# Performance work log

Hardware: AMD Instinct MI355X
Metric: run time of the kernel (lower is better)

The kernel has to match this reference:

```python
import jax, jax.numpy as jnp
import numpy as np

B, N, M, D, H = 2, 512, 512, 128, 256
EPS = 1e-5


def _layernorm(x, g, b):
    mu = jnp.mean(x, axis=-1, keepdims=True)
    var = jnp.mean(jnp.square(x - mu), axis=-1, keepdims=True)
    return (x - mu) * jax.lax.rsqrt(var + EPS) * g + b


def setup_inputs() -> dict:
    key = jax.random.key(0)
    ks = jax.random.split(key, 12)
    X = jax.random.normal(ks[0], (B, N, D), dtype=jnp.float32)
    Y = jax.random.normal(ks[1], (B, M, D), dtype=jnp.float32)
    mask = jax.random.randint(ks[2], (B, N, M), 0, 2).astype(jnp.int32)
    s_in = 1.0 / np.sqrt(2 * D)
    s_h = 1.0 / np.sqrt(H)
    s_d = 1.0 / np.sqrt(D)
    # edge-net Linear(2D, H) split into Y-half and X-half (pairs = cat([Y, X]))
    W1y = jax.random.normal(ks[3], (D, H), dtype=jnp.float32) * s_in
    W1x = jax.random.normal(ks[4], (D, H), dtype=jnp.float32) * s_in
    b1 = jnp.zeros((H,), dtype=jnp.float32)
    W2 = jax.random.normal(ks[5], (H, D), dtype=jnp.float32) * s_h
    b2 = jnp.zeros((D,), dtype=jnp.float32)
    Wf1 = jax.random.normal(ks[6], (D, H), dtype=jnp.float32) * s_d
    bf1 = jnp.zeros((H,), dtype=jnp.float32)
    Wf2 = jax.random.normal(ks[7], (H, D), dtype=jnp.float32) * s_h
    bf2 = jnp.zeros((D,), dtype=jnp.float32)
    g0 = jnp.ones((D,), dtype=jnp.float32)
    be0 = jnp.zeros((D,), dtype=jnp.float32)
    g1 = jnp.ones((D,), dtype=jnp.float32)
    be1 = jnp.zeros((D,), dtype=jnp.float32)
    return {"X": X, "Y": Y, "mask": mask, "W1y": W1y, "W1x": W1x, "b1": b1,
            "W2": W2, "b2": b2, "Wf1": Wf1, "bf1": bf1, "Wf2": Wf2, "bf2": bf2,
            "g0": g0, "be0": be0, "g1": g1, "be1": be1}


def reference(X, Y, mask, W1y, W1x, b1, W2, b2, Wf1, bf1, Wf2, bf2, g0, be0, g1, be1):
    # pairs[b,n,m] = concat(Y[b,m], X[b,n]); Linear on concat == sum of two GEMMs,
    # so avoid materializing the [B,N,M,2D] pairs tensor.
    hy = jnp.einsum('bmd,dh->bmh', Y, W1y)          # [B,M,H]
    hx = jnp.einsum('bnd,dh->bnh', X, W1x)          # [B,N,H]
    h = jax.nn.relu(hy[:, None, :, :] + hx[:, :, None, :] + b1)   # [B,N,M,H]
    E = jnp.einsum('bnmh,hd->bnmd', h, W2) + b2     # [B,N,M,D]
    E = E * mask[..., None].astype(E.dtype)         # masked sum-pool over M
    Z = X + jnp.sum(E, axis=2)                      # residual, [B,N,D]
    Z = _layernorm(Z, g0, be0)
    Z = Z + jax.nn.relu(Z @ Wf1 + bf1) @ Wf2 + bf2  # residual MLP
    Z = _layernorm(Z, g1, be1)
    return Z
```

## Files before the change

kernel.cpp:

```cpp
#include <hip/hip_runtime.h>

#define BB 2
#define NN 512
#define MM 512
#define DD 128
#define HH 256

__global__ __launch_bounds__(256) void k_inproj(
    const float* __restrict__ X, const float* __restrict__ Y,
    const float* __restrict__ W1x, const float* __restrict__ W1y,
    const float* __restrict__ b1,
    float* __restrict__ hx, float* __restrict__ hy)
{
    __shared__ float sr[DD][8];
    int blk = blockIdx.x;
    bool isX = blk < 128;
    const float* src = isX ? X : Y;
    const float* W   = isX ? W1x : W1y;
    float* dst       = isX ? hx : hy;
    int row0 = (isX ? blk : blk - 128) * 8;
    int t = threadIdx.x;

    for (int k = 0; k < 4; ++k) {
        int idx = t + k * 256;
        int r = idx >> 7, d = idx & 127;
        sr[d][r] = src[(row0 + r) * DD + d];
    }
    __syncthreads();

    float bias = isX ? b1[t] : 0.0f;
    float acc[8];
#pragma unroll
    for (int i = 0; i < 8; ++i) acc[i] = bias;

    for (int d = 0; d < DD; ++d) {
        float w = W[d * HH + t];
        float4 a0 = *(const float4*)&sr[d][0];
        float4 a1 = *(const float4*)&sr[d][4];
        acc[0] = fmaf(a0.x, w, acc[0]);
        acc[1] = fmaf(a0.y, w, acc[1]);
        acc[2] = fmaf(a0.z, w, acc[2]);
        acc[3] = fmaf(a0.w, w, acc[3]);
        acc[4] = fmaf(a1.x, w, acc[4]);
        acc[5] = fmaf(a1.y, w, acc[5]);
        acc[6] = fmaf(a1.z, w, acc[6]);
        acc[7] = fmaf(a1.w, w, acc[7]);
    }
#pragma unroll
    for (int i = 0; i < 8; ++i) dst[(row0 + i) * HH + t] = acc[i];
}

__global__ __launch_bounds__(256) void k_main(
    const float* __restrict__ hx, const float* __restrict__ hy,
    const int* __restrict__ mask, float* __restrict__ Spart)
{
    __shared__ float mf[256][4];
    int blk   = blockIdx.x;
    int ms    = blk & 1;
    int ntile = (blk >> 1) & 127;
    int b     = blk >> 8;
    int n0    = ntile * 4;
    int t     = threadIdx.x;

    const int* mrow = mask + (b * NN + n0) * MM + ms * 256;
#pragma unroll
    for (int i = 0; i < 4; ++i)
        mf[t][i] = (float)mrow[i * MM + t];
    __syncthreads();

    float hxv[4], acc[4] = {0.f, 0.f, 0.f, 0.f};
#pragma unroll
    for (int i = 0; i < 4; ++i)
        hxv[i] = hx[(b * NN + n0 + i) * HH + t];

    const float* hyp = hy + (b * MM + ms * 256) * HH + t;
#pragma unroll 4
    for (int m = 0; m < 256; ++m) {
        float hyv = hyp[m * HH];
        float4 m4 = *(const float4*)&mf[m][0];
        float t0 = fmaxf(hxv[0] + hyv, 0.f);
        float t1 = fmaxf(hxv[1] + hyv, 0.f);
        float t2 = fmaxf(hxv[2] + hyv, 0.f);
        float t3 = fmaxf(hxv[3] + hyv, 0.f);
        acc[0] = fmaf(t0, m4.x, acc[0]);
        acc[1] = fmaf(t1, m4.y, acc[1]);
        acc[2] = fmaf(t2, m4.z, acc[2]);
        acc[3] = fmaf(t3, m4.w, acc[3]);
    }
    float* sp = Spart + (size_t)ms * (BB * NN * HH) + (b * NN + n0) * HH + t;
#pragma unroll
    for (int i = 0; i < 4; ++i) sp[i * HH] = acc[i];
}

__global__ __launch_bounds__(256) void k_epi(
    const float* __restrict__ X, const int* __restrict__ mask,
    const float* __restrict__ Spart,
    const float* __restrict__ W2, const float* __restrict__ b2,
    const float* __restrict__ Wf1, const float* __restrict__ bf1,
    const float* __restrict__ Wf2, const float* __restrict__ bf2,
    const float* __restrict__ g0, const float* __restrict__ be0,
    const float* __restrict__ g1, const float* __restrict__ be1,
    float* __restrict__ out)
{
    __shared__ float sS[4][HH];
    __shared__ float szp[4][DD];
    __shared__ float sz[4][DD];
    __shared__ float su[4][HH];
    __shared__ float spart[2][4][DD];
    __shared__ float scnt[4];

    int blk = blockIdx.x;
    int b   = blk >> 7;
    int n0  = (blk & 127) * 4;
    int t   = threadIdx.x;
    int wave = t >> 6, lane = t & 63;

#pragma unroll
    for (int i = 0; i < 4; ++i)
        sS[i][t] = Spart[(b * NN + n0 + i) * HH + t]
                 + Spart[(size_t)(BB * NN * HH) + (b * NN + n0 + i) * HH + t];

    {
        const int* mrow = mask + (b * NN + n0 + wave) * MM;
        int c = 0;
#pragma unroll
        for (int k = 0; k < 8; ++k) c += mrow[lane + k * 64];
#pragma unroll
        for (int off = 32; off; off >>= 1) c += __shfl_down(c, off);
        if (lane == 0) scnt[wave] = (float)c;
    }
    __syncthreads();

    {
        int d = t & 127, half = t >> 7;
        float a0 = 0, a1 = 0, a2 = 0, a3 = 0;
        int hbase = half * 128;
        for (int h = 0; h < 128; ++h) {
            float w = W2[(hbase + h) * DD + d];
            a0 = fmaf(sS[0][hbase + h], w, a0);
            a1 = fmaf(sS[1][hbase + h], w, a1);
            a2 = fmaf(sS[2][hbase + h], w, a2);
            a3 = fmaf(sS[3][hbase + h], w, a3);
        }
        spart[half][0][d] = a0; spart[half][1][d] = a1;
        spart[half][2][d] = a2; spart[half][3][d] = a3;
    }
    __syncthreads();
#pragma unroll
    for (int k = 0; k < 2; ++k) {
        int o = t + k * 256, i = o >> 7, d = o & 127;
        szp[i][d] = spart[0][i][d] + spart[1][i][d]
                  + X[(b * NN + n0 + i) * DD + d] + scnt[i] * b2[d];
    }
    __syncthreads();

    {
        float v0 = szp[wave][lane], v1 = szp[wave][lane + 64];
        float s = v0 + v1, q = v0 * v0 + v1 * v1;
#pragma unroll
        for (int off = 32; off; off >>= 1) { s += __shfl_down(s, off); q += __shfl_down(q, off); }
        s = __shfl(s, 0); q = __shfl(q, 0);
        float mu   = s * (1.0f / 128.0f);
        float var  = q * (1.0f / 128.0f) - mu * mu;
        float rstd = rsqrtf(var + 1e-5f);
        sz[wave][lane]      = (v0 - mu) * rstd * g0[lane]      + be0[lane];
        sz[wave][lane + 64] = (v1 - mu) * rstd * g0[lane + 64] + be0[lane + 64];
    }
    __syncthreads();

    {
        float bias = bf1[t];
        float a0 = bias, a1 = bias, a2 = bias, a3 = bias;
        for (int d = 0; d < DD; ++d) {
            float w = Wf1[d * HH + t];
            a0 = fmaf(sz[0][d], w, a0);
            a1 = fmaf(sz[1][d], w, a1);
            a2 = fmaf(sz[2][d], w, a2);
            a3 = fmaf(sz[3][d], w, a3);
        }
        su[0][t] = fmaxf(a0, 0.f);
        su[1][t] = fmaxf(a1, 0.f);
        su[2][t] = fmaxf(a2, 0.f);
        su[3][t] = fmaxf(a3, 0.f);
    }
    __syncthreads();

    {
        int d = t & 127, half = t >> 7;
        float a0 = 0, a1 = 0, a2 = 0, a3 = 0;
        int hbase = half * 128;
        for (int h = 0; h < 128; ++h) {
            float w = Wf2[(hbase + h) * DD + d];
            a0 = fmaf(su[0][hbase + h], w, a0);
            a1 = fmaf(su[1][hbase + h], w, a1);
            a2 = fmaf(su[2][hbase + h], w, a2);
            a3 = fmaf(su[3][hbase + h], w, a3);
        }
        spart[half][0][d] = a0; spart[half][1][d] = a1;
        spart[half][2][d] = a2; spart[half][3][d] = a3;
    }
    __syncthreads();
#pragma unroll
    for (int k = 0; k < 2; ++k) {
        int o = t + k * 256, i = o >> 7, d = o & 127;
        szp[i][d] = sz[i][d] + spart[0][i][d] + spart[1][i][d] + bf2[d];
    }
    __syncthreads();

    {
        float v0 = szp[wave][lane], v1 = szp[wave][lane + 64];
        float s = v0 + v1, q = v0 * v0 + v1 * v1;
#pragma unroll
        for (int off = 32; off; off >>= 1) { s += __shfl_down(s, off); q += __shfl_down(q, off); }
        s = __shfl(s, 0); q = __shfl(q, 0);
        float mu   = s * (1.0f / 128.0f);
        float var  = q * (1.0f / 128.0f) - mu * mu;
        float rstd = rsqrtf(var + 1e-5f);
        int row = (b * NN + n0 + wave) * DD;
        out[row + lane]      = (v0 - mu) * rstd * g1[lane]      + be1[lane];
        out[row + lane + 64] = (v1 - mu) * rstd * g1[lane + 64] + be1[lane + 64];
    }
}

extern "C" void kernel_launch(void* const* d_in, const int* in_sizes, int n_in,
                              void* d_out, int out_size, void* d_ws, size_t ws_size,
                              hipStream_t stream)
{
    const float* X    = (const float*)d_in[0];
    const float* Y    = (const float*)d_in[1];
    const int*   mask = (const int*)d_in[2];
    const float* W1y  = (const float*)d_in[3];
    const float* W1x  = (const float*)d_in[4];
    const float* b1   = (const float*)d_in[5];
    const float* W2   = (const float*)d_in[6];
    const float* b2   = (const float*)d_in[7];
    const float* Wf1  = (const float*)d_in[8];
    const float* bf1  = (const float*)d_in[9];
    const float* Wf2  = (const float*)d_in[10];
    const float* bf2  = (const float*)d_in[11];
    const float* g0   = (const float*)d_in[12];
    const float* be0  = (const float*)d_in[13];
    const float* g1   = (const float*)d_in[14];
    const float* be1  = (const float*)d_in[15];
    float* out = (float*)d_out;

    float* ws = (float*)d_ws;
    float* hx = ws;
    float* hy = ws + BB * NN * HH;
    float* Sp = ws + 2 * BB * NN * HH;

    k_inproj<<<256, 256, 0, stream>>>(X, Y, W1x, W1y, b1, hx, hy);
    k_main  <<<512, 256, 0, stream>>>(hx, hy, mask, Sp);
    k_epi   <<<256, 256, 0, stream>>>(X, mask, Sp, W2, b2, Wf1, bf1, Wf2, bf2,
                                      g0, be0, g1, be1, out);
}
```

Before: 135.4 us.

## Split work finer across all three kernels to raise block and thread counts

The input projection now computes 4 rows per block instead of 8, doubling the block count. The main pairwise reduction splits M into four chunks instead of two, doubling its blocks. The epilogue uses 512 threads and splits each reduction dimension across more thread groups, combining the pieces through a shared scratch buffer. The aim is more waves in flight to hide latency on a many-CU GPU, at the cost of more partial-sum traffic and a larger workspace for the four Spart slices.

```diff
diff --git a/kernel.cpp b/kernel.cpp
--- a/kernel.cpp
+++ b/kernel.cpp
@@ -12,16 +12,17 @@
     const float* __restrict__ b1,
     float* __restrict__ hx, float* __restrict__ hy)
 {
-    __shared__ float sr[DD][8];
+    __shared__ float sr[DD][4];
     int blk = blockIdx.x;
-    bool isX = blk < 128;
+    bool isX = blk < 256;
     const float* src = isX ? X : Y;
     const float* W   = isX ? W1x : W1y;
     float* dst       = isX ? hx : hy;
-    int row0 = (isX ? blk : blk - 128) * 8;
+    int row0 = (isX ? blk : blk - 256) * 4;
     int t = threadIdx.x;
 
-    for (int k = 0; k < 4; ++k) {
+#pragma unroll
+    for (int k = 0; k < 2; ++k) {
         int idx = t + k * 256;
         int r = idx >> 7, d = idx & 127;
         sr[d][r] = src[(row0 + r) * DD + d];
@@ -29,43 +30,41 @@
     __syncthreads();
 
     float bias = isX ? b1[t] : 0.0f;
-    float acc[8];
-#pragma unroll
-    for (int i = 0; i < 8; ++i) acc[i] = bias;
-
+    float a0 = bias, a1 = bias, a2 = bias, a3 = bias;
+
+#pragma unroll 16
     for (int d = 0; d < DD; ++d) {
         float w = W[d * HH + t];
-        float4 a0 = *(const float4*)&sr[d][0];
-        float4 a1 = *(const float4*)&sr[d][4];
-        acc[0] = fmaf(a0.x, w, acc[0]);
-        acc[1] = fmaf(a0.y, w, acc[1]);
-        acc[2] = fmaf(a0.z, w, acc[2]);
-        acc[3] = fmaf(a0.w, w, acc[3]);
-        acc[4] = fmaf(a1.x, w, acc[4]);
-        acc[5] = fmaf(a1.y, w, acc[5]);
-        acc[6] = fmaf(a1.z, w, acc[6]);
-        acc[7] = fmaf(a1.w, w, acc[7]);
-    }
-#pragma unroll
-    for (int i = 0; i < 8; ++i) dst[(row0 + i) * HH + t] = acc[i];
+        float4 a = *(const float4*)&sr[d][0];
+        a0 = fmaf(a.x, w, a0);
+        a1 = fmaf(a.y, w, a1);
+        a2 = fmaf(a.z, w, a2);
+        a3 = fmaf(a.w, w, a3);
+    }
+    dst[(row0 + 0) * HH + t] = a0;
+    dst[(row0 + 1) * HH + t] = a1;
+    dst[(row0 + 2) * HH + t] = a2;
+    dst[(row0 + 3) * HH + t] = a3;
 }
 
 __global__ __launch_bounds__(256) void k_main(
     const float* __restrict__ hx, const float* __restrict__ hy,
     const int* __restrict__ mask, float* __restrict__ Spart)
 {
-    __shared__ float mf[256][4];
+    __shared__ float mf[128][4];
     int blk   = blockIdx.x;
-    int ms    = blk & 1;
-    int ntile = (blk >> 1) & 127;
-    int b     = blk >> 8;
+    int ms    = blk & 3;
+    int ntile = (blk >> 2) & 127;
+    int b     = blk >> 9;
     int n0    = ntile * 4;
     int t     = threadIdx.x;
 
-    const int* mrow = mask + (b * NN + n0) * MM + ms * 256;
-#pragma unroll
-    for (int i = 0; i < 4; ++i)
-        mf[t][i] = (float)mrow[i * MM + t];
+    if (t < 128) {
+        const int* mrow = mask + (b * NN + n0) * MM + ms * 128 + t;
+#pragma unroll
+        for (int i = 0; i < 4; ++i)
+            mf[t][i] = (float)mrow[i * MM];
+    }
     __syncthreads();
 
     float hxv[4], acc[4] = {0.f, 0.f, 0.f, 0.f};
@@ -73,9 +72,9 @@
     for (int i = 0; i < 4; ++i)
         hxv[i] = hx[(b * NN + n0 + i) * HH + t];
 
-    const float* hyp = hy + (b * MM + ms * 256) * HH + t;
-#pragma unroll 4
-    for (int m = 0; m < 256; ++m) {
+    const float* hyp = hy + (b * MM + ms * 128) * HH + t;
+#pragma unroll 8
+    for (int m = 0; m < 128; ++m) {
         float hyv = hyp[m * HH];
         float4 m4 = *(const float4*)&mf[m][0];
         float t0 = fmaxf(hxv[0] + hyv, 0.f);
@@ -92,7 +91,7 @@
     for (int i = 0; i < 4; ++i) sp[i * HH] = acc[i];
 }
 
-__global__ __launch_bounds__(256) void k_epi(
+__global__ __launch_bounds__(512) void k_epi(
     const float* __restrict__ X, const int* __restrict__ mask,
     const float* __restrict__ Spart,
     const float* __restrict__ W2, const float* __restrict__ b2,
@@ -106,7 +105,7 @@
     __shared__ float szp[4][DD];
     __shared__ float sz[4][DD];
     __shared__ float su[4][HH];
-    __shared__ float spart[2][4][DD];
+    __shared__ float scratch[2048];
     __shared__ float scnt[4];
 
     int blk = blockIdx.x;
@@ -116,11 +115,17 @@
     int wave = t >> 6, lane = t & 63;
 
 #pragma unroll
-    for (int i = 0; i < 4; ++i)
-        sS[i][t] = Spart[(b * NN + n0 + i) * HH + t]
-                 + Spart[(size_t)(BB * NN * HH) + (b * NN + n0 + i) * HH + t];
-
-    {
+    for (int k = 0; k < 2; ++k) {
+        int idx = t + k * 512;
+        int r = idx >> 8, h = idx & 255;
+        size_t base = (size_t)(b * NN + n0 + r) * HH + h;
+        sS[r][h] = Spart[base]
+                 + Spart[base + (size_t)1 * BB * NN * HH]
+                 + Spart[base + (size_t)2 * BB * NN * HH]
+                 + Spart[base + (size_t)3 * BB * NN * HH];
+    }
+
+    if (wave < 4) {
         const int* mrow = mask + (b * NN + n0 + wave) * MM;
         int c = 0;
 #pragma unroll
@@ -132,29 +137,30 @@
     __syncthreads();
 
     {
-        int d = t & 127, half = t >> 7;
+        int d = t & 127, q = t >> 7;
         float a0 = 0, a1 = 0, a2 = 0, a3 = 0;
-        int hbase = half * 128;
-        for (int h = 0; h < 128; ++h) {
+        int hbase = q * 64;
+#pragma unroll 8
+        for (int h = 0; h < 64; ++h) {
             float w = W2[(hbase + h) * DD + d];
             a0 = fmaf(sS[0][hbase + h], w, a0);
             a1 = fmaf(sS[1][hbase + h], w, a1);
             a2 = fmaf(sS[2][hbase + h], w, a2);
             a3 = fmaf(sS[3][hbase + h], w, a3);
         }
-        spart[half][0][d] = a0; spart[half][1][d] = a1;
-        spart[half][2][d] = a2; spart[half][3][d] = a3;
-    }
-    __syncthreads();
-#pragma unroll
-    for (int k = 0; k < 2; ++k) {
-        int o = t + k * 256, i = o >> 7, d = o & 127;
-        szp[i][d] = spart[0][i][d] + spart[1][i][d]
-                  + X[(b * NN + n0 + i) * DD + d] + scnt[i] * b2[d];
-    }
-    __syncthreads();
-
-    {
+        float* sp = scratch + (q * 4) * DD + d;
+        sp[0 * DD] = a0; sp[1 * DD] = a1; sp[2 * DD] = a2; sp[3 * DD] = a3;
+    }
+    __syncthreads();
+    {
+        int r = t >> 7, d = t & 127;
+        szp[r][d] = scratch[(0 * 4 + r) * DD + d] + scratch[(1 * 4 + r) * DD + d]
+                  + scratch[(2 * 4 + r) * DD + d] + scratch[(3 * 4 + r) * DD + d]
+                  + X[(b * NN + n0 + r) * DD + d] + scnt[r] * b2[d];
+    }
+    __syncthreads();
+
+    if (wave < 4) {
         float v0 = szp[wave][lane], v1 = szp[wave][lane + 64];
         float s = v0 + v1, q = v0 * v0 + v1 * v1;
 #pragma unroll
@@ -169,45 +175,55 @@
     __syncthreads();
 
     {
-        float bias = bf1[t];
-        float a0 = bias, a1 = bias, a2 = bias, a3 = bias;
-        for (int d = 0; d < DD; ++d) {
-            float w = Wf1[d * HH + t];
-            a0 = fmaf(sz[0][d], w, a0);
-            a1 = fmaf(sz[1][d], w, a1);
-            a2 = fmaf(sz[2][d], w, a2);
-            a3 = fmaf(sz[3][d], w, a3);
+        int h = t & 255, dh = t >> 8;
+        float a0 = 0, a1 = 0, a2 = 0, a3 = 0;
+        int dbase = dh * 64;
+#pragma unroll 8
+        for (int d = 0; d < 64; ++d) {
+            float w = Wf1[(dbase + d) * HH + h];
+            a0 = fmaf(sz[0][dbase + d], w, a0);
+            a1 = fmaf(sz[1][dbase + d], w, a1);
+            a2 = fmaf(sz[2][dbase + d], w, a2);
+            a3 = fmaf(sz[3][dbase + d], w, a3);
         }
-        su[0][t] = fmaxf(a0, 0.f);
-        su[1][t] = fmaxf(a1, 0.f);
-        su[2][t] = fmaxf(a2, 0.f);
-        su[3][t] = fmaxf(a3, 0.f);
-    }
-    __syncthreads();
-
-    {
-        int d = t & 127, half = t >> 7;
+        float* sp = scratch + (dh * 4) * HH + h;
+        sp[0 * HH] = a0; sp[1 * HH] = a1; sp[2 * HH] = a2; sp[3 * HH] = a3;
+    }
+    __syncthreads();
+#pragma unroll
+    for (int k = 0; k < 2; ++k) {
+        int idx = t + k * 512;
+        int r = idx >> 8, h = idx & 255;
+        su[r][h] = fmaxf(scratch[(0 * 4 + r) * HH + h]
+                       + scratch[(1 * 4 + r) * HH + h] + bf1[h], 0.f);
+    }
+    __syncthreads();
+
+    {
+        int d = t & 127, q = t >> 7;
         float a0 = 0, a1 = 0, a2 = 0, a3 = 0;
-        int hbase = half * 128;
-        for (int h = 0; h < 128; ++h) {
+        int hbase = q * 64;
+#pragma unroll 8
+        for (int h = 0; h < 64; ++h) {
             float w = Wf2[(hbase + h) * DD + d];
             a0 = fmaf(su[0][hbase + h], w, a0);
             a1 = fmaf(su[1][hbase + h], w, a1);
             a2 = fmaf(su[2][hbase + h], w, a2);
             a3 = fmaf(su[3][hbase + h], w, a3);
         }
-        spart[half][0][d] = a0; spart[half][1][d] = a1;
-        spart[half][2][d] = a2; spart[half][3][d] = a3;
-    }
-    __syncthreads();
-#pragma unroll
-    for (int k = 0; k < 2; ++k) {
-        int o = t + k * 256, i = o >> 7, d = o & 127;
-        szp[i][d] = sz[i][d] + spart[0][i][d] + spart[1][i][d] + bf2[d];
-    }
-    __syncthreads();
-
-    {
+        float* sp = scratch + (q * 4) * DD + d;
+        sp[0 * DD] = a0; sp[1 * DD] = a1; sp[2 * DD] = a2; sp[3 * DD] = a3;
+    }
+    __syncthreads();
+    {
+        int r = t >> 7, d = t & 127;
+        szp[r][d] = sz[r][d] + bf2[d]
+                  + scratch[(0 * 4 + r) * DD + d] + scratch[(1 * 4 + r) * DD + d]
+                  + scratch[(2 * 4 + r) * DD + d] + scratch[(3 * 4 + r) * DD + d];
+    }
+    __syncthreads();
+
+    if (wave < 4) {
         float v0 = szp[wave][lane], v1 = szp[wave][lane + 64];
         float s = v0 + v1, q = v0 * v0 + v1 * v1;
 #pragma unroll
@@ -249,8 +265,8 @@
     float* hy = ws + BB * NN * HH;
     float* Sp = ws + 2 * BB * NN * HH;
 
-    k_inproj<<<256, 256, 0, stream>>>(X, Y, W1x, W1y, b1, hx, hy);
-    k_main  <<<512, 256, 0, stream>>>(hx, hy, mask, Sp);
-    k_epi   <<<256, 256, 0, stream>>>(X, mask, Sp, W2, b2, Wf1, bf1, Wf2, bf2,
+    k_inproj<<<512, 256, 0, stream>>>(X, Y, W1x, W1y, b1, hx, hy);
+    k_main  <<<1024, 256, 0, stream>>>(hx, hy, mask, Sp);
+    k_epi   <<<256, 512, 0, stream>>>(X, mask, Sp, W2, b2, Wf1, bf1, Wf2, bf2,
                                       g0, be0, g1, be1, out);
 }
```

Result: faster. 117.2 us (-13.5%).
